# Kernel optimization log

Measured on AMD Instinct MI355X. Metric: run time of the kernel, lower is better.

## Reference

```python
import jax, jax.numpy as jnp
import numpy as np

K = 3      # kernel_size
PAD = 1    # padding


def setup_inputs() -> dict:
    key = jax.random.key(0)
    ks = jax.random.split(key, 5)
    B, Cin, Cout, H, W = 8, 64, 64, 128, 128
    x = jax.random.normal(ks[0], (B, Cin, H, W), jnp.float32)
    # offset conv params (zero-init in the module; use small random values so the
    # deformable gather path is actually exercised)
    offset_w = jax.random.normal(ks[1], (2 * K, Cin, K, K), jnp.float32) * 0.01
    offset_b = jax.random.normal(ks[2], (2 * K,), jnp.float32) * 0.01
    # kaiming-normal strip weights
    std = float(np.sqrt(2.0 / (Cin * K)))
    w_h = jax.random.normal(ks[3], (Cout, Cin, 1, K), jnp.float32) * std
    w_v = jax.random.normal(ks[4], (Cout, Cin, K, 1), jnp.float32) * std
    return {"x": x, "offset_w": offset_w, "offset_b": offset_b, "w_h": w_h, "w_v": w_v}


def _bilinear_gather(x, py, px):
    # x: [B,C,H,W]; py, px: [B,K,H,W] float sampling coordinates.
    # Returns bilinearly sampled values [B,C,K,H,W] with zero padding outside.
    B, C, H, W = x.shape
    y0 = jnp.floor(py)
    x0 = jnp.floor(px)
    wy1 = py - y0
    wx1 = px - x0

    def corner(yf, xf, w):
        valid = ((yf >= 0) & (yf <= H - 1) & (xf >= 0) & (xf <= W - 1)).astype(x.dtype)
        yi = jnp.clip(yf, 0, H - 1).astype(jnp.int32)
        xi = jnp.clip(xf, 0, W - 1).astype(jnp.int32)
        v = jax.vmap(lambda im, yy, xx: im[:, yy, xx])(x, yi, xi)  # [B,C,K,H,W]
        return v * (w * valid)[:, None]

    return (corner(y0, x0, (1 - wy1) * (1 - wx1))
            + corner(y0, x0 + 1, (1 - wy1) * wx1)
            + corner(y0 + 1, x0, wy1 * (1 - wx1))
            + corner(y0 + 1, x0 + 1, wy1 * wx1))


def reference(x, offset_w, offset_b, w_h, w_v):
    B, C, H, W = x.shape
    # offset conv (standard 3x3, stride 1, pad 1) -> [B, 2K, H, W]
    off = jax.lax.conv_general_dilated(
        x, offset_w, window_strides=(1, 1), padding=((PAD, PAD), (PAD, PAD)),
        dimension_numbers=("NCHW", "OIHW", "NCHW")) + offset_b[None, :, None, None]
    h_off = off[:, :K]   # per-tap vertical (y) offsets for the horizontal strip
    v_off = off[:, K:]   # per-tap horizontal (x) offsets for the vertical strip

    ygrid = jnp.arange(H, dtype=x.dtype)
    xgrid = jnp.arange(W, dtype=x.dtype)
    taps = jnp.arange(K, dtype=x.dtype) - PAD  # tap displacements along the strip

    # horizontal strip: taps move along x, deform offsets bend the strip in y
    py_h = ygrid[None, None, :, None] + h_off                              # [B,K,H,W]
    px_h = jnp.broadcast_to(xgrid[None, None, None, :] + taps[None, :, None, None],
                            (B, K, H, W))
    val_h = _bilinear_gather(x, py_h, px_h)                                # [B,C,K,H,W]
    out_h = jnp.einsum("bckhw,ock->bohw", val_h, w_h[:, :, 0, :])

    # vertical strip: taps move along y, deform offsets bend the strip in x
    py_v = jnp.broadcast_to(ygrid[None, None, :, None] + taps[None, :, None, None],
                            (B, K, H, W))
    px_v = xgrid[None, None, None, :] + v_off
    val_v = _bilinear_gather(x, py_v, px_v)
    out_v = jnp.einsum("bckhw,ock->bohw", val_v, w_v[:, :, :, 0])

    return out_h + out_v
```

## Files before the change

### kernel.cpp

```cpp
#include <hip/hip_runtime.h>

#define HH 128
#define WW 128
#define HW (HH * WW)
#define CIN 64
#define COUT 64

#define XT_OFF  0
#define BF_OFF  16777216
#define OBF_OFF (BF_OFF + 49152)

typedef short bf16x8 __attribute__((ext_vector_type(8)));
typedef float f32x4 __attribute__((ext_vector_type(4)));

__device__ __forceinline__ unsigned short f2bf(float f) {
    union { float f; unsigned int u; } v; v.f = f;
    unsigned int r = v.u + 0x7FFFu + ((v.u >> 16) & 1u);
    return (unsigned short)(r >> 16);
}
__device__ __forceinline__ unsigned short f2bf_up(float f) {
    union { float f; unsigned int u; } v; v.f = f;
    return (unsigned short)((v.u + 0x8000u) >> 16);
}
__device__ __forceinline__ float bf2f(unsigned short u) {
    union { unsigned int u; float f; } v; v.u = ((unsigned int)u) << 16;
    return v.f;
}

__global__ __launch_bounds__(256) void prep_repack_kernel(const float* __restrict__ x,
                                                          const float* __restrict__ ow,
                                                          const float* __restrict__ wh,
                                                          const float* __restrict__ wv,
                                                          unsigned short* __restrict__ xT,
                                                          unsigned short* __restrict__ Bf,
                                                          unsigned short* __restrict__ OBf) {
    __shared__ float tile[64 * 129];
    const int tid = threadIdx.x;
    const int blk = blockIdx.x;

    if (blk < 1024) {
        const int b = blk & 7;
        const int y = blk >> 3;
        const float* xb = x + (size_t)b * CIN * HW + y * WW;
        const int tx = tid & 127;
        const int th = tid >> 7;
        for (int c0 = 0; c0 < 64; c0 += 2) {
            int c = c0 + th;
            tile[c * 129 + tx] = xb[(size_t)c * HW + tx];
        }
        __syncthreads();
        unsigned short* ob = xT + ((size_t)b * HW + y * WW) * 64;
#pragma unroll
        for (int it = 0; it < 4; ++it) {
            int e  = it * 256 + tid;
            int h  = e & 7;
            int px = e >> 3;
            union { unsigned short us[8]; uint4 u4; } pkd;
#pragma unroll
            for (int j = 0; j < 8; ++j)
                pkd.us[j] = f2bf(tile[(h * 8 + j) * 129 + px]);
            *(uint4*)&ob[px * 64 + h * 8] = pkd.u4;
        }
    } else {
        int i = (blk - 1024) * 256 + tid;
        if (i < 24576) {
            int j    = i & 7;
            int lane = (i >> 3) & 63;
            int nt   = (i >> 9) & 3;
            int kc   = (i >> 11) & 1;
            int pk   = i >> 12;
            int o = nt * 16 + (lane & 15);
            int c = kc * 32 + (lane >> 4) * 8 + j;
            int k = pk % 3;
            const float* src = (pk < 3) ? wh : wv;
            Bf[i] = f2bf(src[(o * CIN + c) * 3 + k]);
        } else if (i < 24576 + 9216) {
            int mI   = i - 24576;
            int j    = mI & 7;
            int lane = (mI >> 3) & 63;
            int s    = mI >> 9;
            int n    = lane & 15;
            int q    = lane >> 4;
            int c    = (s & 1) * 32 + q * 8 + j;
            int tap  = s >> 1;
            int dy   = tap / 3, dx = tap % 3;
            OBf[mI] = (n < 6) ? f2bf(ow[((n * CIN + c) * 3 + dy) * 3 + dx])
                              : (unsigned short)0;
        }
    }
}

__global__ __launch_bounds__(256, 3) void fused_kernel(const unsigned short* __restrict__ xT,
                                                       const float* __restrict__ obias,
                                                       const unsigned short* __restrict__ Bf,
                                                       const unsigned short* __restrict__ OBf,
                                                       float* __restrict__ out) {
    __shared__ unsigned short BfL[24576];
    __shared__ float offT[4 * 16 * 8];

    const int tid  = threadIdx.x;
    const int w    = tid >> 6;
    const int lane = tid & 63;
    const int q    = lane >> 4;
    const int m    = lane & 15;

    const int blk = blockIdx.x;
    const int b   = blk & 7;
    const int y   = (blk >> 3) & 127;
    const int xh  = blk >> 10;
    const int x0w = (xh << 6) + (w << 4);

    const unsigned short* xtb = xT + (size_t)b * HW * 64;

#pragma unroll
    for (int i = 0; i < 12; ++i)
        *(uint4*)&BfL[(i * 256 + tid) * 8] = ((const uint4*)Bf)[i * 256 + tid];

    f32x4 acc6 = {0.f, 0.f, 0.f, 0.f};
#pragma unroll
    for (int half = 0; half < 2; ++half) {
        const int coff = half * 32 + q * 8;
        uint4 r1[9];
        bool  okt[9];
#pragma unroll
        for (int tap = 0; tap < 9; ++tap) {
            int dy = tap / 3 - 1, dx = tap % 3 - 1;
            int yy = y + dy;
            int xx = x0w + m + dx;
            okt[tap] = (yy >= 0) && (yy < HH) && (xx >= 0) && (xx < WW);
            int yc = min(max(yy, 0), HH - 1);
            int xc = min(max(xx, 0), WW - 1);
            r1[tap] = *(const uint4*)&xtb[(size_t)(yc * WW + xc) * 64 + coff];
        }
#pragma unroll
        for (int tap = 0; tap < 9; ++tap) {
            uint4 raw = okt[tap] ? r1[tap] : make_uint4(0, 0, 0, 0);
            union { uint4 u4; bf16x8 v; } af; af.u4 = raw;
            bf16x8 bfr = *(const bf16x8*)&OBf[((tap * 2 + half) * 64 + lane) * 8];
            acc6 = __builtin_amdgcn_mfma_f32_16x16x32_bf16(af.v, bfr, acc6, 0, 0, 0);
        }
    }
    if (m < 6) {
        float bias = obias[m];
#pragma unroll
        for (int reg = 0; reg < 4; ++reg)
            offT[(w * 16 + q * 4 + reg) * 8 + m] = acc6[reg] + bias;
    }
    __syncthreads();
    f32x4  o03 = *(const f32x4*)&offT[(w * 16 + m) * 8];
    float2 o45 = *(const float2*)&offT[(w * 16 + m) * 8 + 4];
    float offs[6] = {o03[0], o03[1], o03[2], o03[3], o45.x, o45.y};

    const int xs = x0w + m;
    float wA[6], wB[6];
    int   iA[6], iB[6];
#pragma unroll
    for (int pk = 0; pk < 6; ++pk) {
        const int ph = pk / 3;
        const int k  = pk % 3;
        float o1 = offs[pk];
        if (ph == 0) {
            float py  = (float)y + o1;
            float y0f = floorf(py);
            float wy  = py - y0f;
            int   yi  = (int)y0f;
            bool v0 = (yi >= 0) && (yi <= HH - 1);
            bool v1 = (yi + 1 >= 0) && (yi + 1 <= HH - 1);
            int  pxx = xs + k - 1;
            bool pv  = (pxx >= 0) && (pxx <= WW - 1);
            wA[pk] = (pv && v0) ? (1.f - wy) : 0.f;
            wB[pk] = (pv && v1) ? wy : 0.f;
            int ra = min(max(yi, 0), HH - 1);
            int rb = min(max(yi + 1, 0), HH - 1);
            int ca = min(max(pxx, 0), WW - 1);
            iA[pk] = ra * WW + ca;
            iB[pk] = rb * WW + ca;
        } else {
            float pxf = (float)xs + o1;
            float x0f = floorf(pxf);
            float wx  = pxf - x0f;
            int   xi  = (int)x0f;
            bool v0 = (xi >= 0) && (xi <= WW - 1);
            bool v1 = (xi + 1 >= 0) && (xi + 1 <= WW - 1);
            int  py = y + k - 1;
            bool pv = (py >= 0) && (py <= HH - 1);
            wA[pk] = (pv && v0) ? (1.f - wx) : 0.f;
            wB[pk] = (pv && v1) ? wx : 0.f;
            int ra  = min(max(py, 0), HH - 1);
            int ca  = min(max(xi, 0), WW - 1);
            int cb2 = min(max(xi + 1, 0), WW - 1);
            iA[pk] = ra * WW + ca;
            iB[pk] = ra * WW + cb2;
        }
    }

    uint4 rA[12], rB[12];
#pragma unroll
    for (int pk = 0; pk < 6; ++pk) {
#pragma unroll
        for (int kc = 0; kc < 2; ++kc) {
            const int coff = kc * 32 + q * 8;
            rA[pk * 2 + kc] = *(const uint4*)&xtb[(size_t)iA[pk] * 64 + coff];
            rB[pk * 2 + kc] = *(const uint4*)&xtb[(size_t)iB[pk] * 64 + coff];
        }
    }

    f32x4 acc[4];
#pragma unroll
    for (int nt = 0; nt < 4; ++nt) acc[nt] = (f32x4){0.f, 0.f, 0.f, 0.f};

#pragma unroll
    for (int pk = 0; pk < 6; ++pk) {
#pragma unroll
        for (int kc = 0; kc < 2; ++kc) {
            const int g = pk * 2 + kc;
            union { uint4 u4; unsigned short us[8]; } ua, ub;
            ua.u4 = rA[g];
            ub.u4 = rB[g];
            union { unsigned short us[8]; bf16x8 v; } uf;
#pragma unroll
            for (int j = 0; j < 8; ++j) {
                float v = wA[pk] * bf2f(ua.us[j]) + wB[pk] * bf2f(ub.us[j]);
                uf.us[j] = f2bf_up(v);
            }
#pragma unroll
            for (int nt = 0; nt < 4; ++nt) {
                bf16x8 bfr = *(const bf16x8*)&BfL[((g * 4 + nt) * 64 + lane) * 8];
                acc[nt] = __builtin_amdgcn_mfma_f32_16x16x32_bf16(uf.v, bfr, acc[nt], 0, 0, 0);
            }
        }
    }

#pragma unroll
    for (int nt = 0; nt < 4; ++nt) {
        int o = nt * 16 + m;
        float* op = out + ((size_t)(b * COUT + o) * HH + y) * WW + x0w + q * 4;
        *(f32x4*)op = acc[nt];
    }
}

extern "C" void kernel_launch(void* const* d_in, const int* in_sizes, int n_in,
                              void* d_out, int out_size, void* d_ws, size_t ws_size,
                              hipStream_t stream) {
    const float* x     = (const float*)d_in[0];
    const float* ow    = (const float*)d_in[1];
    const float* obias = (const float*)d_in[2];
    const float* wh    = (const float*)d_in[3];
    const float* wv    = (const float*)d_in[4];
    float* out = (float*)d_out;

    char* ws = (char*)d_ws;
    unsigned short* xT  = (unsigned short*)(ws + XT_OFF);
    unsigned short* Bf  = (unsigned short*)(ws + BF_OFF);
    unsigned short* OBf = (unsigned short*)(ws + OBF_OFF);

    prep_repack_kernel<<<dim3(1156), dim3(256), 0, stream>>>(x, ow, wh, wv, xT, Bf, OBf);
    fused_kernel<<<dim3(2048), dim3(256), 0, stream>>>(xT, obias, Bf, OBf, out);
}
```

Measured before the change: 137.7 us.

## Drop LDS weight staging, read weights from global, raise occupancy target

The fused kernel no longer copies the 48KB packed weight matrix into shared memory and instead reads MFMA B fragments directly from global memory, relying on L1/L2 caching. The batched prefetch of gathered xT rows into 24 registers is replaced by loads issued inside the MFMA loop, and launch bounds move from 3 to 4 blocks per SM. The prep kernel's x transpose load is vectorized to float4. The aim is less LDS use, fewer registers and higher occupancy, at the cost of losing load batching and taking more global traffic per MFMA.

```diff
diff --git a/kernel.cpp b/kernel.cpp
--- a/kernel.cpp
+++ b/kernel.cpp
@@ -42,11 +42,14 @@
         const int b = blk & 7;
         const int y = blk >> 3;
         const float* xb = x + (size_t)b * CIN * HW + y * WW;
-        const int tx = tid & 127;
-        const int th = tid >> 7;
-        for (int c0 = 0; c0 < 64; c0 += 2) {
-            int c = c0 + th;
-            tile[c * 129 + tx] = xb[(size_t)c * HW + tx];
+#pragma unroll
+        for (int i = 0; i < 8; ++i) {
+            int idx = i * 256 + tid;
+            int c   = idx >> 5;
+            int px4 = idx & 31;
+            f32x4 v = *(const f32x4*)&xb[(size_t)c * HW + px4 * 4];
+            float* tp = &tile[c * 129 + px4 * 4];
+            tp[0] = v[0]; tp[1] = v[1]; tp[2] = v[2]; tp[3] = v[3];
         }
         __syncthreads();
         unsigned short* ob = xT + ((size_t)b * HW + y * WW) * 64;
@@ -90,12 +93,11 @@
     }
 }
 
-__global__ __launch_bounds__(256, 3) void fused_kernel(const unsigned short* __restrict__ xT,
+__global__ __launch_bounds__(256, 4) void fused_kernel(const unsigned short* __restrict__ xT,
                                                        const float* __restrict__ obias,
                                                        const unsigned short* __restrict__ Bf,
                                                        const unsigned short* __restrict__ OBf,
                                                        float* __restrict__ out) {
-    __shared__ unsigned short BfL[24576];
     __shared__ float offT[4 * 16 * 8];
 
     const int tid  = threadIdx.x;
@@ -111,10 +113,6 @@
     const int x0w = (xh << 6) + (w << 4);
 
     const unsigned short* xtb = xT + (size_t)b * HW * 64;
-
-#pragma unroll
-    for (int i = 0; i < 12; ++i)
-        *(uint4*)&BfL[(i * 256 + tid) * 8] = ((const uint4*)Bf)[i * 256 + tid];
 
     f32x4 acc6 = {0.f, 0.f, 0.f, 0.f};
 #pragma unroll
@@ -194,17 +192,6 @@
         }
     }
 
-    uint4 rA[12], rB[12];
-#pragma unroll
-    for (int pk = 0; pk < 6; ++pk) {
-#pragma unroll
-        for (int kc = 0; kc < 2; ++kc) {
-            const int coff = kc * 32 + q * 8;
-            rA[pk * 2 + kc] = *(const uint4*)&xtb[(size_t)iA[pk] * 64 + coff];
-            rB[pk * 2 + kc] = *(const uint4*)&xtb[(size_t)iB[pk] * 64 + coff];
-        }
-    }
-
     f32x4 acc[4];
 #pragma unroll
     for (int nt = 0; nt < 4; ++nt) acc[nt] = (f32x4){0.f, 0.f, 0.f, 0.f};
@@ -214,9 +201,10 @@
 #pragma unroll
         for (int kc = 0; kc < 2; ++kc) {
             const int g = pk * 2 + kc;
+            const int coff = kc * 32 + q * 8;
             union { uint4 u4; unsigned short us[8]; } ua, ub;
-            ua.u4 = rA[g];
-            ub.u4 = rB[g];
+            ua.u4 = *(const uint4*)&xtb[(size_t)iA[pk] * 64 + coff];
+            ub.u4 = *(const uint4*)&xtb[(size_t)iB[pk] * 64 + coff];
             union { unsigned short us[8]; bf16x8 v; } uf;
 #pragma unroll
             for (int j = 0; j < 8; ++j) {
@@ -225,7 +213,7 @@
             }
 #pragma unroll
             for (int nt = 0; nt < 4; ++nt) {
-                bf16x8 bfr = *(const bf16x8*)&BfL[((g * 4 + nt) * 64 + lane) * 8];
+                bf16x8 bfr = *(const bf16x8*)&Bf[((g * 4 + nt) * 64 + lane) * 8];
                 acc[nt] = __builtin_amdgcn_mfma_f32_16x16x32_bf16(uf.v, bfr, acc[nt], 0, 0, 0);
             }
         }
```

Result: slower. 142.3 us (+3.3%).
